# Performance work log

Hardware: AMD Instinct MI355X
Metric: run time of the kernel (lower is better)

## Reference

```python
import jax, jax.numpy as jnp
import numpy as np

H = 32  # hidden size (hardcoded in source module)

def setup_inputs() -> dict:
    key = jax.random.key(0)
    ks = jax.random.split(key, 7)
    s = 1.0 / np.sqrt(H)  # PyTorch LSTM/Linear init scale
    return {
        "x":    jax.random.normal(ks[0], (8192, 512, 1), dtype=jnp.float32),
        "W_ih": jax.random.uniform(ks[1], (4 * H, 1), minval=-s, maxval=s, dtype=jnp.float32),
        "W_hh": jax.random.uniform(ks[2], (4 * H, H), minval=-s, maxval=s, dtype=jnp.float32),
        "b_ih": jax.random.uniform(ks[3], (4 * H,), minval=-s, maxval=s, dtype=jnp.float32),
        "b_hh": jax.random.uniform(ks[4], (4 * H,), minval=-s, maxval=s, dtype=jnp.float32),
        "W_fc": jax.random.uniform(ks[5], (1, H), minval=-s, maxval=s, dtype=jnp.float32),
        "b_fc": jax.random.uniform(ks[6], (1,), minval=-s, maxval=s, dtype=jnp.float32),
    }

def reference(x, W_ih, W_hh, b_ih, b_hh, W_fc, b_fc):
    B = x.shape[0]
    # Precompute input projections for all timesteps: [B, T, 4H]
    xg = jnp.einsum('bti,gi->btg', x, W_ih) + (b_ih + b_hh)
    xg_t = jnp.swapaxes(xg, 0, 1)  # [T, B, 4H] for scan over time

    def step(carry, xgt):
        h, c = carry
        gates = xgt + h @ W_hh.T           # [B, 4H]
        i, f, g, o = jnp.split(gates, 4, axis=-1)  # PyTorch gate order i,f,g,o
        i = jax.nn.sigmoid(i)
        f = jax.nn.sigmoid(f)
        g = jnp.tanh(g)
        o = jax.nn.sigmoid(o)
        c = f * c + i * g
        h = o * jnp.tanh(c)
        return (h, c), None

    h0 = jnp.zeros((B, H), dtype=x.dtype)
    c0 = jnp.zeros((B, H), dtype=x.dtype)
    (h_last, _), _ = jax.lax.scan(step, (h0, c0), xg_t)
    # Final linear head on last timestep hidden state: [B, output_size]
    return h_last @ W_fc.T + b_fc
```

## Files before the change

### kernel.cpp

```cpp
#include <hip/hip_runtime.h>


#define TT 512
#define HH 32
#define L2E 1.44269504088896340736f

typedef _Float16 f16x8 __attribute__((ext_vector_type(8)));
typedef __fp16 fp16x2 __attribute__((ext_vector_type(2)));
typedef float f32x4 __attribute__((ext_vector_type(4)));
typedef float f32x2 __attribute__((ext_vector_type(2)));

__device__ __forceinline__ float fastrcp(float x) { return __builtin_amdgcn_rcpf(x); }
__device__ __forceinline__ float exp2f_(float x) { return __builtin_amdgcn_exp2f(x); }

#define XROW 132

__launch_bounds__(256, 2)
__global__ void lstm_kernel(const float* __restrict__ x,
                            const float* __restrict__ W_ih,
                            const float* __restrict__ W_hh,
                            const float* __restrict__ b_ih,
                            const float* __restrict__ b_hh,
                            const float* __restrict__ W_fc,
                            const float* __restrict__ b_fc,
                            float* __restrict__ out) {
    __shared__ _Float16 hhp[2][512];
    __shared__ _Float16 hlp[2][512];
    __shared__ float xbuf[16 * XROW];

    const int tid  = threadIdx.x;
    const int lane = tid & 63;
    const int w    = tid >> 6;
    const int c    = lane & 15;
    const int q    = lane >> 4;
    const int base = blockIdx.x * 16;

    const int gate = c & 3;
    const float asc = (gate == 2) ? (2.0f * L2E) : (-L2E);
    const int wrow0 = gate * 32 + 8 * (c >> 2);
    f16x8 wah[2];
    #pragma unroll
    for (int tt = 0; tt < 2; ++tt) {
        const int t8 = 2 * w + tt;
        #pragma unroll
        for (int j = 0; j < 8; ++j) {
            const int u = 8 * q + (j ^ (2 * q));
            wah[tt][j] = (_Float16)(W_hh[(wrow0 + t8) * HH + u] * asc);
        }
    }

    f32x4 wihs[2], bcs[2];
    #pragma unroll
    for (int tt = 0; tt < 2; ++tt) {
        const int u = 8 * q + 2 * w + tt;
        #pragma unroll
        for (int r = 0; r < 4; ++r) {
            const float sc = (r == 2) ? (2.0f * L2E) : (-L2E);
            wihs[tt][r] = W_ih[32 * r + u] * sc;
            bcs[tt][r]  = (b_ih[32 * r + u] + b_hh[32 * r + u]) * sc;
        }
    }

    #pragma unroll
    for (int i = tid; i < 512; i += 256) {
        hhp[0][i] = (_Float16)0.f;
        hlp[0][i] = (_Float16)0.f;
    }

    f32x2 cs2 = {0.f, 0.f};

    const int xrow = tid >> 4;
    const int xj4  = (tid & 15) * 4;

    const int rdo = q * 128 + c * 8;
    const int wro = rdo + ((2 * w) ^ (2 * q));

    #define STEP(t, RP, WP)                                                   \
    {                                                                         \
        const f16x8 bh = *(const f16x8*)&hhp[RP][rdo];                        \
        const f16x8 bl = *(const f16x8*)&hlp[RP][rdo];                        \
        const float xc = xbuf[c * XROW + ((t) & 127)];                        \
        f32x4 acc[2];                                                         \
        _Pragma("unroll")                                                     \
        for (int tt = 0; tt < 2; ++tt) {                                      \
            f32x4 a = wihs[tt] * xc + bcs[tt];                                \
            a = __builtin_amdgcn_mfma_f32_16x16x32_f16(wah[tt], bh, a, 0,0,0);\
            a = __builtin_amdgcn_mfma_f32_16x16x32_f16(wah[tt], bl, a, 0,0,0);\
            acc[tt] = a;                                                      \
        }                                                                     \
        f32x2 Ei, Ef, G, Eo;                                                  \
        Ei.x = exp2f_(acc[0][0]); Ei.y = exp2f_(acc[1][0]);                   \
        Ef.x = exp2f_(acc[0][1]); Ef.y = exp2f_(acc[1][1]);                   \
        G.x  = exp2f_(acc[0][2]); G.y  = exp2f_(acc[1][2]);                   \
        Eo.x = exp2f_(acc[0][3]); Eo.y = exp2f_(acc[1][3]);                   \
        const f32x2 one = {1.f, 1.f};                                         \
        const f32x2 aig = (one + Ei) * (G + one);                             \
        const f32x2 af  = one + Ef;                                           \
        const f32x2 num = cs2 * aig + (G - one) * af;                         \
        const f32x2 den = af * aig;                                           \
        f32x2 rc; rc.x = fastrcp(den.x); rc.y = fastrcp(den.y);               \
        const f32x2 cn = num * rc;                                            \
        cs2 = cn;                                                             \
        f32x2 yc = cn * (2.0f * L2E);                                         \
        yc.x = fminf(60.f, fmaxf(-60.f, yc.x));                               \
        yc.y = fminf(60.f, fmaxf(-60.f, yc.y));                               \
        f32x2 C; C.x = exp2f_(yc.x); C.y = exp2f_(yc.y);                      \
        const f32x2 hden = (C + one) * (one + Eo);                            \
        f32x2 hr; hr.x = fastrcp(hden.x); hr.y = fastrcp(hden.y);             \
        const f32x2 hv = (C - one) * hr;                                      \
        union { fp16x2 v; int i; _Float16 e[2]; } ph, pl;                     \
        ph.v = __builtin_amdgcn_cvt_pkrtz(hv.x, hv.y);                        \
        pl.v = __builtin_amdgcn_cvt_pkrtz(hv.x - (float)ph.e[0],              \
                                          hv.y - (float)ph.e[1]);             \
        *(int*)&hhp[WP][wro] = ph.i;                                          \
        *(int*)&hlp[WP][wro] = pl.i;                                          \
        __syncthreads();                                                      \
    }

    for (int t = 0; t < TT; t += 2) {
        if ((t & 127) == 0) {
            #pragma unroll
            for (int s = 0; s < 2; ++s) {
                const float4 v = *(const float4*)&x[(base + xrow) * TT + t + xj4 + 64 * s];
                *(float4*)&xbuf[xrow * XROW + xj4 + 64 * s] = v;
            }
            __syncthreads();
        }
        STEP(t,     0, 1);
        STEP(t + 1, 1, 0);
    }

    if (tid < 16) {
        float s = b_fc[0];
        #pragma unroll
        for (int u = 0; u < 32; ++u) {
            const int qb = u >> 3;
            const int off = qb * 128 + tid * 8 + ((u & 7) ^ (2 * qb));
            s += ((float)hhp[0][off] + (float)hlp[0][off]) * W_fc[u];
        }
        out[base + tid] = s;
    }
}

extern "C" void kernel_launch(void* const* d_in, const int* in_sizes, int n_in,
                              void* d_out, int out_size, void* d_ws, size_t ws_size,
                              hipStream_t stream) {
    const float* x    = (const float*)d_in[0];
    const float* W_ih = (const float*)d_in[1];
    const float* W_hh = (const float*)d_in[2];
    const float* b_ih = (const float*)d_in[3];
    const float* b_hh = (const float*)d_in[4];
    const float* W_fc = (const float*)d_in[5];
    const float* b_fc = (const float*)d_in[6];
    float* out = (float*)d_out;

    const int B = 8192;
    lstm_kernel<<<B / 16, 256, 0, stream>>>(x, W_ih, W_hh, b_ih, b_hh,
                                            W_fc, b_fc, out);
}
```

Before: 247.9 us.

## Halve block to two waves, each computing four MFMA tiles per step

Each block now runs 128 threads (2 waves) instead of 256, and each wave handles four 16-row gate tiles per timestep instead of two. The hidden-state exchange buffer moves from two separate swizzled fp16 arrays to one padded interleaved hi/lo array, so each lane reads both B operands from its own row. This halves the number of waves taking part in the per-step barrier and gives each wave more independent MFMAs and transcendental ops to overlap. In exchange each wave carries more registers and a longer serial chain per step, and there are fewer waves per block to hide latency.

```diff
diff --git a/kernel.cpp b/kernel.cpp
--- a/kernel.cpp
+++ b/kernel.cpp
@@ -4,18 +4,16 @@
 #define TT 512
 #define HH 32
 #define L2E 1.44269504088896340736f
+#define XROW 132
 
 typedef _Float16 f16x8 __attribute__((ext_vector_type(8)));
 typedef __fp16 fp16x2 __attribute__((ext_vector_type(2)));
 typedef float f32x4 __attribute__((ext_vector_type(4)));
-typedef float f32x2 __attribute__((ext_vector_type(2)));
 
 __device__ __forceinline__ float fastrcp(float x) { return __builtin_amdgcn_rcpf(x); }
 __device__ __forceinline__ float exp2f_(float x) { return __builtin_amdgcn_exp2f(x); }
 
-#define XROW 132
-
-__launch_bounds__(256, 2)
+__launch_bounds__(128)
 __global__ void lstm_kernel(const float* __restrict__ x,
                             const float* __restrict__ W_ih,
                             const float* __restrict__ W_hh,
@@ -24,8 +22,7 @@
                             const float* __restrict__ W_fc,
                             const float* __restrict__ b_fc,
                             float* __restrict__ out) {
-    __shared__ _Float16 hhp[2][512];
-    __shared__ _Float16 hlp[2][512];
+    __shared__ int hx[2][64][12];
     __shared__ float xbuf[16 * XROW];
 
     const int tid  = threadIdx.x;
@@ -38,107 +35,122 @@
     const int gate = c & 3;
     const float asc = (gate == 2) ? (2.0f * L2E) : (-L2E);
     const int wrow0 = gate * 32 + 8 * (c >> 2);
-    f16x8 wah[2];
+    f16x8 wa[4];
     #pragma unroll
-    for (int tt = 0; tt < 2; ++tt) {
-        const int t8 = 2 * w + tt;
+    for (int tt = 0; tt < 4; ++tt) {
+        const int t8 = 4 * w + tt;
         #pragma unroll
-        for (int j = 0; j < 8; ++j) {
-            const int u = 8 * q + (j ^ (2 * q));
-            wah[tt][j] = (_Float16)(W_hh[(wrow0 + t8) * HH + u] * asc);
+        for (int j = 0; j < 8; ++j)
+            wa[tt][j] = (_Float16)(W_hh[(wrow0 + t8) * HH + 8 * q + j] * asc);
+    }
+
+    f32x4 wih[4], bcs[4];
+    #pragma unroll
+    for (int tt = 0; tt < 4; ++tt) {
+        const int u = 8 * q + 4 * w + tt;
+        #pragma unroll
+        for (int r = 0; r < 4; ++r) {
+            const float sc = (r == 2) ? (2.0f * L2E) : (-L2E);
+            wih[tt][r] = W_ih[32 * r + u] * sc;
+            bcs[tt][r] = (b_ih[32 * r + u] + b_hh[32 * r + u]) * sc;
         }
     }
 
-    f32x4 wihs[2], bcs[2];
-    #pragma unroll
-    for (int tt = 0; tt < 2; ++tt) {
-        const int u = 8 * q + 2 * w + tt;
-        #pragma unroll
-        for (int r = 0; r < 4; ++r) {
-            const float sc = (r == 2) ? (2.0f * L2E) : (-L2E);
-            wihs[tt][r] = W_ih[32 * r + u] * sc;
-            bcs[tt][r]  = (b_ih[32 * r + u] + b_hh[32 * r + u]) * sc;
-        }
+    {
+        int2 z; z.x = 0; z.y = 0;
+        *(int2*)&hx[0][lane][2 * w]     = z;
+        *(int2*)&hx[0][lane][4 + 2 * w] = z;
     }
 
-    #pragma unroll
-    for (int i = tid; i < 512; i += 256) {
-        hhp[0][i] = (_Float16)0.f;
-        hlp[0][i] = (_Float16)0.f;
-    }
+    f32x4 cs = {0.f, 0.f, 0.f, 0.f};
 
-    f32x2 cs2 = {0.f, 0.f};
+    const int xrow = tid >> 3;
+    const int xcol = (tid & 7) * 4;
 
-    const int xrow = tid >> 4;
-    const int xj4  = (tid & 15) * 4;
+    auto step = [&](int t, int RP, int WP) {
+        const f16x8 BH = *(const f16x8*)&hx[RP][lane][0];
+        const f16x8 BL = *(const f16x8*)&hx[RP][lane][4];
+        const float xc = xbuf[c * XROW + (t & 127)];
+        f32x4 acc[4];
+        #pragma unroll
+        for (int tt = 0; tt < 4; ++tt) {
+            f32x4 a = wih[tt] * xc + bcs[tt];
+            acc[tt] = __builtin_amdgcn_mfma_f32_16x16x32_f16(wa[tt], BH, a, 0, 0, 0);
+        }
+        #pragma unroll
+        for (int tt = 0; tt < 4; ++tt)
+            acc[tt] = __builtin_amdgcn_mfma_f32_16x16x32_f16(wa[tt], BL, acc[tt], 0, 0, 0);
 
-    const int rdo = q * 128 + c * 8;
-    const int wro = rdo + ((2 * w) ^ (2 * q));
+        f32x4 Ei, Ef, G, Eo;
+        #pragma unroll
+        for (int tt = 0; tt < 4; ++tt) {
+            Ei[tt] = exp2f_(acc[tt][0]);
+            Ef[tt] = exp2f_(acc[tt][1]);
+            G[tt]  = exp2f_(acc[tt][2]);
+            Eo[tt] = exp2f_(acc[tt][3]);
+        }
+        const f32x4 one = {1.f, 1.f, 1.f, 1.f};
+        const f32x4 aig = (one + Ei) * (G + one);
+        const f32x4 af  = one + Ef;
+        const f32x4 num = cs * aig + (G - one) * af;
+        const f32x4 den = af * aig;
+        f32x4 rc;
+        #pragma unroll
+        for (int tt = 0; tt < 4; ++tt) rc[tt] = fastrcp(den[tt]);
+        const f32x4 cn = num * rc;
+        cs = cn;
+        f32x4 yc = cn * (2.0f * L2E);
+        #pragma unroll
+        for (int tt = 0; tt < 4; ++tt)
+            yc[tt] = __builtin_amdgcn_fmed3f(yc[tt], -60.f, 60.f);
+        f32x4 C;
+        #pragma unroll
+        for (int tt = 0; tt < 4; ++tt) C[tt] = exp2f_(yc[tt]);
+        const f32x4 hden = (C + one) * (one + Eo);
+        f32x4 hr;
+        #pragma unroll
+        for (int tt = 0; tt < 4; ++tt) hr[tt] = fastrcp(hden[tt]);
+        const f32x4 hv = (C - one) * hr;
 
-    #define STEP(t, RP, WP)                                                   \
-    {                                                                         \
-        const f16x8 bh = *(const f16x8*)&hhp[RP][rdo];                        \
-        const f16x8 bl = *(const f16x8*)&hlp[RP][rdo];                        \
-        const float xc = xbuf[c * XROW + ((t) & 127)];                        \
-        f32x4 acc[2];                                                         \
-        _Pragma("unroll")                                                     \
-        for (int tt = 0; tt < 2; ++tt) {                                      \
-            f32x4 a = wihs[tt] * xc + bcs[tt];                                \
-            a = __builtin_amdgcn_mfma_f32_16x16x32_f16(wah[tt], bh, a, 0,0,0);\
-            a = __builtin_amdgcn_mfma_f32_16x16x32_f16(wah[tt], bl, a, 0,0,0);\
-            acc[tt] = a;                                                      \
-        }                                                                     \
-        f32x2 Ei, Ef, G, Eo;                                                  \
-        Ei.x = exp2f_(acc[0][0]); Ei.y = exp2f_(acc[1][0]);                   \
-        Ef.x = exp2f_(acc[0][1]); Ef.y = exp2f_(acc[1][1]);                   \
-        G.x  = exp2f_(acc[0][2]); G.y  = exp2f_(acc[1][2]);                   \
-        Eo.x = exp2f_(acc[0][3]); Eo.y = exp2f_(acc[1][3]);                   \
-        const f32x2 one = {1.f, 1.f};                                         \
-        const f32x2 aig = (one + Ei) * (G + one);                             \
-        const f32x2 af  = one + Ef;                                           \
-        const f32x2 num = cs2 * aig + (G - one) * af;                         \
-        const f32x2 den = af * aig;                                           \
-        f32x2 rc; rc.x = fastrcp(den.x); rc.y = fastrcp(den.y);               \
-        const f32x2 cn = num * rc;                                            \
-        cs2 = cn;                                                             \
-        f32x2 yc = cn * (2.0f * L2E);                                         \
-        yc.x = fminf(60.f, fmaxf(-60.f, yc.x));                               \
-        yc.y = fminf(60.f, fmaxf(-60.f, yc.y));                               \
-        f32x2 C; C.x = exp2f_(yc.x); C.y = exp2f_(yc.y);                      \
-        const f32x2 hden = (C + one) * (one + Eo);                            \
-        f32x2 hr; hr.x = fastrcp(hden.x); hr.y = fastrcp(hden.y);             \
-        const f32x2 hv = (C - one) * hr;                                      \
-        union { fp16x2 v; int i; _Float16 e[2]; } ph, pl;                     \
-        ph.v = __builtin_amdgcn_cvt_pkrtz(hv.x, hv.y);                        \
-        pl.v = __builtin_amdgcn_cvt_pkrtz(hv.x - (float)ph.e[0],              \
-                                          hv.y - (float)ph.e[1]);             \
-        *(int*)&hhp[WP][wro] = ph.i;                                          \
-        *(int*)&hlp[WP][wro] = pl.i;                                          \
-        __syncthreads();                                                      \
-    }
+        union PK { fp16x2 v; int i; _Float16 e[2]; };
+        PK h01, h23, l01, l23;
+        h01.v = __builtin_amdgcn_cvt_pkrtz(hv[0], hv[1]);
+        h23.v = __builtin_amdgcn_cvt_pkrtz(hv[2], hv[3]);
+        int2 whi; whi.x = h01.i; whi.y = h23.i;
+        *(int2*)&hx[WP][lane][2 * w] = whi;
+        l01.v = __builtin_amdgcn_cvt_pkrtz(hv[0] - (float)h01.e[0],
+                                           hv[1] - (float)h01.e[1]);
+        l23.v = __builtin_amdgcn_cvt_pkrtz(hv[2] - (float)h23.e[0],
+                                           hv[3] - (float)h23.e[1]);
+        int2 wlo; wlo.x = l01.i; wlo.y = l23.i;
+        *(int2*)&hx[WP][lane][4 + 2 * w] = wlo;
+        __syncthreads();
+    };
 
     for (int t = 0; t < TT; t += 2) {
         if ((t & 127) == 0) {
             #pragma unroll
-            for (int s = 0; s < 2; ++s) {
-                const float4 v = *(const float4*)&x[(base + xrow) * TT + t + xj4 + 64 * s];
-                *(float4*)&xbuf[xrow * XROW + xj4 + 64 * s] = v;
+            for (int s = 0; s < 4; ++s) {
+                const float4 v = *(const float4*)&x[(base + xrow) * TT + t + xcol + 32 * s];
+                *(float4*)&xbuf[xrow * XROW + xcol + 32 * s] = v;
             }
             __syncthreads();
         }
-        STEP(t,     0, 1);
-        STEP(t + 1, 1, 0);
+        step(t,     0, 1);
+        step(t + 1, 1, 0);
     }
 
-    if (tid < 16) {
-        float s = b_fc[0];
+    {
+        const f16x8 BH = *(const f16x8*)&hx[0][lane][0];
+        const f16x8 BL = *(const f16x8*)&hx[0][lane][4];
+        float s = 0.f;
         #pragma unroll
-        for (int u = 0; u < 32; ++u) {
-            const int qb = u >> 3;
-            const int off = qb * 128 + tid * 8 + ((u & 7) ^ (2 * qb));
-            s += ((float)hhp[0][off] + (float)hlp[0][off]) * W_fc[u];
-        }
-        out[base + tid] = s;
+        for (int j = 0; j < 8; ++j)
+            s += ((float)BH[j] + (float)BL[j]) * W_fc[8 * q + j];
+        s += __shfl_xor(s, 16);
+        s += __shfl_xor(s, 32);
+        if (tid < 16)
+            out[base + tid] = b_fc[0] + s;
     }
 }
 
@@ -155,6 +167,6 @@
     float* out = (float*)d_out;
 
     const int B = 8192;
-    lstm_kernel<<<B / 16, 256, 0, stream>>>(x, W_ih, W_hh, b_ih, b_hh,
+    lstm_kernel<<<B / 16, 128, 0, stream>>>(x, W_ih, W_hh, b_ih, b_hh,
                                             W_fc, b_fc, out);
 }
```

New measurement: 419.1 us. 69.0% more time.

## Interleave two batch groups per block to overlap MFMA and elementwise phases

Applied to the files above, without the earlier changes.

Each block now handles two independent 16-row batch groups with 512 threads. The step is split into an MFMA+exp phase and an elementwise cell-update phase, and the two groups are staggered so one group's matrix work runs while the other's elementwise work runs, with setprio raising MFMA priority. The input projection for the next step is precomputed after the state write, and the clamp now uses fmed3. This aims to hide the serial per-step latency of the recurrence, at the cost of more shared memory, a two-barrier-per-step schedule and fewer blocks.

```diff
diff --git a/kernel.cpp b/kernel.cpp
--- a/kernel.cpp
+++ b/kernel.cpp
@@ -4,6 +4,7 @@
 #define TT 512
 #define HH 32
 #define L2E 1.44269504088896340736f
+#define XROW 132
 
 typedef _Float16 f16x8 __attribute__((ext_vector_type(8)));
 typedef __fp16 fp16x2 __attribute__((ext_vector_type(2)));
@@ -13,9 +14,7 @@
 __device__ __forceinline__ float fastrcp(float x) { return __builtin_amdgcn_rcpf(x); }
 __device__ __forceinline__ float exp2f_(float x) { return __builtin_amdgcn_exp2f(x); }
 
-#define XROW 132
-
-__launch_bounds__(256, 2)
+__launch_bounds__(512, 2)
 __global__ void lstm_kernel(const float* __restrict__ x,
                             const float* __restrict__ W_ih,
                             const float* __restrict__ W_hh,
@@ -24,16 +23,19 @@
                             const float* __restrict__ W_fc,
                             const float* __restrict__ b_fc,
                             float* __restrict__ out) {
-    __shared__ _Float16 hhp[2][512];
-    __shared__ _Float16 hlp[2][512];
-    __shared__ float xbuf[16 * XROW];
+    __shared__ _Float16 hhp[2][2][512];
+    __shared__ _Float16 hlp[2][2][512];
+    __shared__ float xbuf[2][16 * XROW];
 
     const int tid  = threadIdx.x;
     const int lane = tid & 63;
-    const int w    = tid >> 6;
+    const int wv   = tid >> 6;
+    const int grp  = wv >> 2;
+    const int w    = wv & 3;
     const int c    = lane & 15;
     const int q    = lane >> 4;
-    const int base = blockIdx.x * 16;
+    const int tg   = tid & 255;
+    const int gbase = blockIdx.x * 32 + grp * 16;
 
     const int gate = c & 3;
     const float asc = (gate == 2) ? (2.0f * L2E) : (-L2E);
@@ -62,83 +64,113 @@
     }
 
     #pragma unroll
-    for (int i = tid; i < 512; i += 256) {
-        hhp[0][i] = (_Float16)0.f;
-        hlp[0][i] = (_Float16)0.f;
+    for (int i = tg; i < 512; i += 256) {
+        hhp[grp][0][i] = (_Float16)0.f;
+        hlp[grp][0][i] = (_Float16)0.f;
     }
 
-    f32x2 cs2 = {0.f, 0.f};
-
-    const int xrow = tid >> 4;
-    const int xj4  = (tid & 15) * 4;
+    const int xrow = tg >> 4;
+    const int xj4  = (tg & 15) * 4;
+    #pragma unroll
+    for (int s = 0; s < 2; ++s) {
+        const float4 v = *(const float4*)&x[(size_t)(gbase + xrow) * TT + xj4 + 64 * s];
+        *(float4*)&xbuf[grp][xrow * XROW + xj4 + 64 * s] = v;
+    }
+    __syncthreads();
 
     const int rdo = q * 128 + c * 8;
     const int wro = rdo + ((2 * w) ^ (2 * q));
 
-    #define STEP(t, RP, WP)                                                   \
-    {                                                                         \
-        const f16x8 bh = *(const f16x8*)&hhp[RP][rdo];                        \
-        const f16x8 bl = *(const f16x8*)&hlp[RP][rdo];                        \
-        const float xc = xbuf[c * XROW + ((t) & 127)];                        \
-        f32x4 acc[2];                                                         \
-        _Pragma("unroll")                                                     \
-        for (int tt = 0; tt < 2; ++tt) {                                      \
-            f32x4 a = wihs[tt] * xc + bcs[tt];                                \
-            a = __builtin_amdgcn_mfma_f32_16x16x32_f16(wah[tt], bh, a, 0,0,0);\
-            a = __builtin_amdgcn_mfma_f32_16x16x32_f16(wah[tt], bl, a, 0,0,0);\
-            acc[tt] = a;                                                      \
-        }                                                                     \
-        f32x2 Ei, Ef, G, Eo;                                                  \
-        Ei.x = exp2f_(acc[0][0]); Ei.y = exp2f_(acc[1][0]);                   \
-        Ef.x = exp2f_(acc[0][1]); Ef.y = exp2f_(acc[1][1]);                   \
-        G.x  = exp2f_(acc[0][2]); G.y  = exp2f_(acc[1][2]);                   \
-        Eo.x = exp2f_(acc[0][3]); Eo.y = exp2f_(acc[1][3]);                   \
-        const f32x2 one = {1.f, 1.f};                                         \
-        const f32x2 aig = (one + Ei) * (G + one);                             \
-        const f32x2 af  = one + Ef;                                           \
-        const f32x2 num = cs2 * aig + (G - one) * af;                         \
-        const f32x2 den = af * aig;                                           \
-        f32x2 rc; rc.x = fastrcp(den.x); rc.y = fastrcp(den.y);               \
-        const f32x2 cn = num * rc;                                            \
-        cs2 = cn;                                                             \
-        f32x2 yc = cn * (2.0f * L2E);                                         \
-        yc.x = fminf(60.f, fmaxf(-60.f, yc.x));                               \
-        yc.y = fminf(60.f, fmaxf(-60.f, yc.y));                               \
-        f32x2 C; C.x = exp2f_(yc.x); C.y = exp2f_(yc.y);                      \
-        const f32x2 hden = (C + one) * (one + Eo);                            \
-        f32x2 hr; hr.x = fastrcp(hden.x); hr.y = fastrcp(hden.y);             \
-        const f32x2 hv = (C - one) * hr;                                      \
-        union { fp16x2 v; int i; _Float16 e[2]; } ph, pl;                     \
-        ph.v = __builtin_amdgcn_cvt_pkrtz(hv.x, hv.y);                        \
-        pl.v = __builtin_amdgcn_cvt_pkrtz(hv.x - (float)ph.e[0],              \
-                                          hv.y - (float)ph.e[1]);             \
-        *(int*)&hhp[WP][wro] = ph.i;                                          \
-        *(int*)&hlp[WP][wro] = pl.i;                                          \
-        __syncthreads();                                                      \
+    f32x2 cs2 = {0.f, 0.f};
+    f32x2 Ei, Ef, G, Eo;
+    f32x4 ai[2];
+    {
+        const float xc = xbuf[grp][c * XROW];
+        ai[0] = wihs[0] * xc + bcs[0];
+        ai[1] = wihs[1] * xc + bcs[1];
     }
 
-    for (int t = 0; t < TT; t += 2) {
-        if ((t & 127) == 0) {
-            #pragma unroll
-            for (int s = 0; s < 2; ++s) {
-                const float4 v = *(const float4*)&x[(base + xrow) * TT + t + xj4 + 64 * s];
-                *(float4*)&xbuf[xrow * XROW + xj4 + 64 * s] = v;
-            }
-            __syncthreads();
+    auto P1 = [&](int t) {
+        const int RP = t & 1;
+        const f16x8 bh = *(const f16x8*)&hhp[grp][RP][rdo];
+        const f16x8 bl = *(const f16x8*)&hlp[grp][RP][rdo];
+        __builtin_amdgcn_s_setprio(1);
+        f32x4 a0 = __builtin_amdgcn_mfma_f32_16x16x32_f16(wah[0], bh, ai[0], 0, 0, 0);
+        f32x4 a1 = __builtin_amdgcn_mfma_f32_16x16x32_f16(wah[1], bh, ai[1], 0, 0, 0);
+        a0 = __builtin_amdgcn_mfma_f32_16x16x32_f16(wah[0], bl, a0, 0, 0, 0);
+        a1 = __builtin_amdgcn_mfma_f32_16x16x32_f16(wah[1], bl, a1, 0, 0, 0);
+        Ei.x = exp2f_(a0[0]); Ei.y = exp2f_(a1[0]);
+        Ef.x = exp2f_(a0[1]); Ef.y = exp2f_(a1[1]);
+        G.x  = exp2f_(a0[2]); G.y  = exp2f_(a1[2]);
+        Eo.x = exp2f_(a0[3]); Eo.y = exp2f_(a1[3]);
+        __builtin_amdgcn_s_setprio(0);
+    };
+
+    auto P2 = [&](int t) {
+        const int WP = (t & 1) ^ 1;
+        const f32x2 one = {1.f, 1.f};
+        const f32x2 aig = (one + Ei) * (G + one);
+        const f32x2 af  = one + Ef;
+        const f32x2 num = cs2 * aig + (G - one) * af;
+        const f32x2 den = af * aig;
+        f32x2 rc; rc.x = fastrcp(den.x); rc.y = fastrcp(den.y);
+        const f32x2 cn = num * rc;
+        cs2 = cn;
+        f32x2 yc = cn * (2.0f * L2E);
+        yc.x = __builtin_amdgcn_fmed3f(yc.x, -60.f, 60.f);
+        yc.y = __builtin_amdgcn_fmed3f(yc.y, -60.f, 60.f);
+        f32x2 C; C.x = exp2f_(yc.x); C.y = exp2f_(yc.y);
+        const f32x2 hden = (C + one) * (one + Eo);
+        f32x2 hr; hr.x = fastrcp(hden.x); hr.y = fastrcp(hden.y);
+        const f32x2 hv = (C - one) * hr;
+        union PK { fp16x2 v; int i; _Float16 e[2]; } ph, pl;
+        ph.v = __builtin_amdgcn_cvt_pkrtz(hv.x, hv.y);
+        pl.v = __builtin_amdgcn_cvt_pkrtz(hv.x - (float)ph.e[0],
+                                          hv.y - (float)ph.e[1]);
+        *(int*)&hhp[grp][WP][wro] = ph.i;
+        *(int*)&hlp[grp][WP][wro] = pl.i;
+        const float xn = xbuf[grp][c * XROW + ((t + 1) & 127)];
+        ai[0] = wihs[0] * xn + bcs[0];
+        ai[1] = wihs[1] * xn + bcs[1];
+    };
+
+    auto stage = [&](int tc) {
+        #pragma unroll
+        for (int s = 0; s < 2; ++s) {
+            const float4 v = *(const float4*)&x[(size_t)(gbase + xrow) * TT + tc + xj4 + 64 * s];
+            *(float4*)&xbuf[grp][xrow * XROW + xj4 + 64 * s] = v;
         }
-        STEP(t,     0, 1);
-        STEP(t + 1, 1, 0);
+    };
+
+    #pragma unroll 1
+    for (int t = 0; t < TT; ++t) {
+        if (grp == 0) {
+            P1(t);
+            if (((t + 1) & 127) == 0 && (t + 1) < TT) stage(t + 1);
+        } else {
+            if (t) P2(t - 1);
+        }
+        __syncthreads();
+        if (grp == 0) {
+            P2(t);
+        } else {
+            P1(t);
+            if (((t + 1) & 127) == 0 && (t + 1) < TT) stage(t + 1);
+        }
+        __syncthreads();
     }
+    if (grp == 1) P2(TT - 1);
+    __syncthreads();
 
-    if (tid < 16) {
+    if (tg < 16) {
         float s = b_fc[0];
         #pragma unroll
         for (int u = 0; u < 32; ++u) {
             const int qb = u >> 3;
-            const int off = qb * 128 + tid * 8 + ((u & 7) ^ (2 * qb));
-            s += ((float)hhp[0][off] + (float)hlp[0][off]) * W_fc[u];
+            const int off = qb * 128 + tg * 8 + ((u & 7) ^ (2 * qb));
+            s += ((float)hhp[grp][0][off] + (float)hlp[grp][0][off]) * W_fc[u];
         }
-        out[base + tid] = s;
+        out[gbase + tg] = s;
     }
 }
 
@@ -155,6 +187,6 @@
     float* out = (float*)d_out;
 
     const int B = 8192;
-    lstm_kernel<<<B / 16, 256, 0, stream>>>(x, W_ih, W_hh, b_ih, b_hh,
+    lstm_kernel<<<B / 32, 512, 0, stream>>>(x, W_ih, W_hh, b_ih, b_hh,
                                             W_fc, b_fc, out);
 }
```

Result: slower. 351.5 us (+41.8%).
